# Performance work log

Hardware: AMD Instinct MI355X
Metric: run time of the kernel (lower is better)

The kernel has to match this reference:

```python
import jax, jax.numpy as jnp
import numpy as np

C = 32
KSHAPE = (C, C, 3, 3)  # (C_out, C_in, kH, kW)
BN_EPS = 1e-5


def _binary_act(x):
    # forward: sign(x); backward: identity clipped to |x|<1 (STE)
    xc = jnp.clip(x, -1.0, 1.0)
    return jax.lax.stop_gradient(jnp.sign(x) - xc) + xc


def _binarize_weight(w_flat, shape):
    w = w_flat.reshape(shape)
    scale = jax.lax.stop_gradient(jnp.mean(jnp.abs(w)))  # global scalar scale, detached
    wc = jnp.clip(w, -1.0, 1.0)
    # forward: scale*sign(w); backward flows through clamp(w,-1,1)
    return jax.lax.stop_gradient(scale * jnp.sign(w) - wc) + wc


def _bi_conv_bn(x, w_flat, gamma, beta, stride):
    xb = _binary_act(x)
    w = _binarize_weight(w_flat, KSHAPE)
    y = jax.lax.conv_general_dilated(
        xb, w, window_strides=(stride, stride), padding=[(1, 1), (1, 1)],
        dimension_numbers=('NCHW', 'OIHW', 'NCHW'))
    # BatchNorm2d in training mode (batch stats, biased variance)
    m = jnp.mean(y, axis=(0, 2, 3), keepdims=True)
    v = jnp.mean((y - m) ** 2, axis=(0, 2, 3), keepdims=True)
    yhat = (y - m) * jax.lax.rsqrt(v + BN_EPS)
    return gamma.reshape(1, -1, 1, 1) * yhat + beta.reshape(1, -1, 1, 1)


def setup_inputs() -> dict:
    key = jax.random.key(0)
    k1, k2, k3 = jax.random.split(key, 3)
    return {
        'x': jax.random.normal(k1, (32, C, 160, 160), dtype=jnp.float32),
        'w1': jax.random.normal(k2, (C * C * 9, 1), dtype=jnp.float32) * 0.05,
        'gamma1': jnp.ones((C,), dtype=jnp.float32),
        'beta1': jnp.zeros((C,), dtype=jnp.float32),
        'w2': jax.random.normal(k3, (C * C * 9, 1), dtype=jnp.float32) * 0.05,
        'gamma2': jnp.ones((C,), dtype=jnp.float32),
        'beta2': jnp.zeros((C,), dtype=jnp.float32),
    }


def reference(x, w1, gamma1, beta1, w2, gamma2, beta2):
    # bireal residual block, stride=1 => skip_op is Identity
    inner = _bi_conv_bn(x, w1, gamma1, beta1, 1) + x
    out = _bi_conv_bn(inner, w2, gamma2, beta2, 1) + inner
    return out
```

## Files before the change

kernel.cpp:

```cpp
#include <hip/hip_runtime.h>
#include <stdint.h>

#define NIMG 32
#define CH 32
#define HH 160
#define WW 160
#define HWL (HH*WW)
#define PRS 164
#define PHH 162
#define PIMG (PHH*PRS)
#define NPIX (NIMG*HWL)
#define HALO_WORDS 968

#define OFF_P     0
#define OFF_P2    3400704
#define OFF_WP    (OFF_P2 + 3400704)
#define OFF_CORR  (OFF_WP + 2304)
#define OFF_SC    (OFF_CORR + 2304)
#define OFF_SB    (OFF_SC + 128)

struct StatLine {
  int s1; int pad0; unsigned long long s2; char pad[112];
};

#define AS1 __attribute__((address_space(1)))
#define AS3 __attribute__((address_space(3)))
__device__ __forceinline__ void dma16(const void* g, void* l) {
  __builtin_amdgcn_global_load_lds((const AS1 void*)g, (AS3 void*)l, 16, 0, 0);
}

__device__ __forceinline__ void conv4(const uint32_t r[3][6], const uint32_t* wsh,
                                      int co, int& a0, int& a1, int& a2, int& a3)
{
  a0 = a1 = a2 = a3 = 0;
  #pragma unroll
  for (int dy = 0; dy < 3; ++dy) {
    #pragma unroll
    for (int dx = 0; dx < 3; ++dx) {
      uint32_t wvv = wsh[co * 9 + dy * 3 + dx];
      a0 += __popc(r[dy][0 + dx] ^ wvv);
      a1 += __popc(r[dy][1 + dx] ^ wvv);
      a2 += __popc(r[dy][2 + dx] ^ wvv);
      a3 += __popc(r[dy][3 + dx] ^ wvv);
    }
  }
}

__global__ __launch_bounds__(256) void pack_prep(const float* __restrict__ x,
    const float* __restrict__ w1, const float* __restrict__ w2,
    uint32_t* __restrict__ P, uint32_t* __restrict__ P2, uint32_t* __restrict__ WP,
    int* __restrict__ CORR, float* __restrict__ SC, StatLine* __restrict__ SB)
{
  __shared__ float lds[8192];
  const int tid = threadIdx.x;
  const int b = blockIdx.x;

  if (b >= 3200) {
    if (b == 3442) {
      int* z = (int*)SB;
      for (int i = tid; i < 2048; i += 256) z[i] = 0;
      float* red = lds;
      uint32_t* wpl = (uint32_t*)(lds + 256);
      for (int cv = 0; cv < 2; ++cv) {
        const float* w = cv ? w2 : w1;
        float s = 0.f;
        #pragma unroll
        for (int j = 0; j < 9; ++j) {
          float4 v = *reinterpret_cast<const float4*>(w + (j * 256 + tid) * 4);
          s += fabsf(v.x) + fabsf(v.y) + fabsf(v.z) + fabsf(v.w);
        }
        red[tid] = s;
        __syncthreads();
        for (int st = 128; st > 0; st >>= 1) {
          if (tid < st) red[tid] += red[tid + st];
          __syncthreads();
        }
        if (tid == 0) SC[cv] = red[0] / 9216.0f;
        for (int i = tid; i < 288; i += 256) {
          int co = i / 9, t = i - co * 9;
          uint32_t bw = 0;
          for (int ci = 0; ci < 32; ++ci)
            bw |= (w[(co * 32 + ci) * 9 + t] > 0.0f) ? (1u << ci) : 0u;
          WP[cv * 288 + i] = bw;
          wpl[i] = bw;
        }
        __syncthreads();
        for (int i = tid; i < 288; i += 256) {
          int cls = i / 32, co = i - cls * 32;
          int hc = cls / 3, wc = cls - hc * 3;
          int corr = 0;
          for (int t = 0; t < 9; ++t) {
            int dy = t / 3 - 1, dx = t % 3 - 1;
            bool inval = (hc == 0 && dy == -1) || (hc == 2 && dy == 1) ||
                         (wc == 0 && dx == -1) || (wc == 2 && dx == 1);
            if (inval) corr += 32 - 2 * __popc(wpl[co * 9 + t]);
          }
          CORR[cv * 288 + cls * 32 + co] = corr;
        }
        __syncthreads();
      }
    } else {
      int k = (b - 3200) * 256 + tid;
      uint32_t* buf = (k < 32 * HALO_WORDS) ? P : P2;
      int j = k % (32 * HALO_WORDS);
      int img = j / HALO_WORDS;
      int r = j - img * HALO_WORDS;
      int pr, pc;
      if (r < 164)      { pr = 0;   pc = r; }
      else if (r < 328) { pr = 161; pc = r - 164; }
      else {
        int k2 = r - 328;
        pr = 1 + (k2 >> 2);
        int q = k2 & 3;
        pc = (q == 0) ? 0 : (160 + q);
      }
      buf[img * PIMG + pr * PRS + pc] = 0;
    }
    return;
  }

  int n = b / 100;
  int p0 = (b - n * 100) * 256;
  const float* xb = x + (size_t)n * CH * HWL + p0;
  #pragma unroll
  for (int it = 0; it < 8; ++it) {
    int c = it * 4 + (tid >> 6);
    dma16(xb + (size_t)c * HWL + (tid & 63) * 4, lds + c * 256);
  }
  __syncthreads();

  uint32_t bits = 0;
  #pragma unroll
  for (int c = 0; c < 32; ++c) {
    if (lds[c * 256 + tid] > 0.f) bits |= 1u << c;
  }
  int px = p0 + tid;
  int h = px / WW, w = px - h * WW;
  P[n * PIMG + (h + 1) * PRS + (w + 1)] = bits;
}

__global__ __launch_bounds__(256) void conv_stats(const uint32_t* __restrict__ P,
    const uint32_t* __restrict__ WP, const int* __restrict__ CORR,
    StatLine* __restrict__ sb)
{
  __shared__ uint32_t wsh[288];
  __shared__ int csh[288];
  __shared__ int ls1[32], ls2[32];
  const int tid = threadIdx.x;
  for (int i = tid; i < 288; i += 256) { wsh[i] = WP[i]; csh[i] = CORR[i]; }
  if (tid < 32) { ls1[tid] = 0; ls2[tid] = 0; }
  __syncthreads();

  int g = blockIdx.x * 256 + tid;
  int w4 = g % 40;
  int t1 = g / 40;
  int h = t1 % 160;
  int n = t1 / 160;

  const uint32_t* base = P + n * PIMG + h * PRS + w4 * 4;
  uint32_t r[3][6];
  #pragma unroll
  for (int dy = 0; dy < 3; ++dy) {
    uint4 a = *reinterpret_cast<const uint4*>(base + dy * PRS);
    uint2 bw = *reinterpret_cast<const uint2*>(base + dy * PRS + 4);
    r[dy][0] = a.x; r[dy][1] = a.y; r[dy][2] = a.z; r[dy][3] = a.w;
    r[dy][4] = bw.x; r[dy][5] = bw.y;
  }

  int rowc = (h == 0) ? 0 : ((h == 159) ? 6 : 3);
  int cls0  = rowc + ((w4 == 0) ? 0 : 1);
  int cls12 = rowc + 1;
  int cls3  = rowc + ((w4 == 39) ? 2 : 1);
  int lane = tid & 63;

  #pragma unroll
  for (int co = 0; co < 32; ++co) {
    int a0, a1, a2, a3;
    conv4(r, wsh, co, a0, a1, a2, a3);
    int d0 = 288 - 2 * a0 - csh[cls0 * 32 + co];
    int d1 = 288 - 2 * a1 - csh[cls12 * 32 + co];
    int d2 = 288 - 2 * a2 - csh[cls12 * 32 + co];
    int d3 = 288 - 2 * a3 - csh[cls3 * 32 + co];
    int ds = d0 + d1 + d2 + d3;
    int sq = d0 * d0 + d1 * d1 + d2 * d2 + d3 * d3;
    #pragma unroll
    for (int off = 32; off > 0; off >>= 1) {
      ds += __shfl_down(ds, off);
      sq += __shfl_down(sq, off);
    }
    if (lane == 0) { atomicAdd(&ls1[co], ds); atomicAdd(&ls2[co], sq); }
  }
  __syncthreads();
  if (tid < 32) {
    atomicAdd(&sb[tid].s1, ls1[tid]);
    atomicAdd(&sb[tid].s2, (unsigned long long)(long long)ls2[tid]);
  }
}

__global__ __launch_bounds__(256, 2) void conv_bn1(const uint32_t* __restrict__ P,
    const uint32_t* __restrict__ WP, const int* __restrict__ CORR,
    const float* __restrict__ x, const float* __restrict__ SCp,
    const StatLine* __restrict__ sb, const float* __restrict__ gamma,
    const float* __restrict__ beta, uint32_t* __restrict__ P2)
{
  __shared__ uint32_t wsh[288];
  __shared__ int csh[288];
  __shared__ float Ash[32], Bsh[32];
  const int tid = threadIdx.x;
  for (int i = tid; i < 288; i += 256) { wsh[i] = WP[i]; csh[i] = CORR[i]; }
  if (tid < 32) {
    double sc = (double)SCp[0];
    double m  = sc * (double)sb[tid].s1 / (double)NPIX;
    double ms = sc * sc * (double)(long long)sb[tid].s2 / (double)NPIX;
    float inv = (float)(1.0 / sqrt(ms - m * m + 1e-5));
    float gm = gamma[tid];
    Ash[tid] = gm * inv * (float)sc;
    Bsh[tid] = beta[tid] - gm * inv * (float)m;
  }
  __syncthreads();

  int g = blockIdx.x * 256 + tid;
  int w4 = g % 40;
  int t1 = g / 40;
  int h = t1 % 160;
  int n = t1 / 160;

  const uint32_t* base = P + n * PIMG + h * PRS + w4 * 4;
  uint32_t r[3][6];
  #pragma unroll
  for (int dy = 0; dy < 3; ++dy) {
    uint4 a = *reinterpret_cast<const uint4*>(base + dy * PRS);
    uint2 bw = *reinterpret_cast<const uint2*>(base + dy * PRS + 4);
    r[dy][0] = a.x; r[dy][1] = a.y; r[dy][2] = a.z; r[dy][3] = a.w;
    r[dy][4] = bw.x; r[dy][5] = bw.y;
  }
  int rowc = (h == 0) ? 0 : ((h == 159) ? 6 : 3);
  int cls0  = rowc + ((w4 == 0) ? 0 : 1);
  int cls12 = rowc + 1;
  int cls3  = rowc + ((w4 == 39) ? 2 : 1);

  int i = h * WW + w4 * 4;
  size_t pbase = (size_t)n * CH * HWL + i;

  uint32_t bb0 = 0, bb1 = 0, bb2 = 0, bb3 = 0;
  #pragma unroll
  for (int cg = 0; cg < 4; ++cg) {
    float4 xv[8];
    #pragma unroll
    for (int j = 0; j < 8; ++j)
      xv[j] = *reinterpret_cast<const float4*>(x + pbase + (size_t)(cg * 8 + j) * HWL);
    #pragma unroll
    for (int j = 0; j < 8; ++j) {
      int co = cg * 8 + j;
      int a0, a1, a2, a3;
      conv4(r, wsh, co, a0, a1, a2, a3);
      int d0 = 288 - 2 * a0 - csh[cls0 * 32 + co];
      int d1 = 288 - 2 * a1 - csh[cls12 * 32 + co];
      int d2 = 288 - 2 * a2 - csh[cls12 * 32 + co];
      int d3 = 288 - 2 * a3 - csh[cls3 * 32 + co];
      float A = Ash[co], Bv = Bsh[co];
      float v0 = fmaf(A, (float)d0, Bv) + xv[j].x;
      float v1 = fmaf(A, (float)d1, Bv) + xv[j].y;
      float v2 = fmaf(A, (float)d2, Bv) + xv[j].z;
      float v3 = fmaf(A, (float)d3, Bv) + xv[j].w;
      uint32_t m = 1u << co;
      if (v0 > 0.f) bb0 |= m;
      if (v1 > 0.f) bb1 |= m;
      if (v2 > 0.f) bb2 |= m;
      if (v3 > 0.f) bb3 |= m;
    }
  }
  uint32_t* pw = P2 + n * PIMG + (h + 1) * PRS + (w4 * 4 + 1);
  pw[0] = bb0; pw[1] = bb1; pw[2] = bb2; pw[3] = bb3;
}

__global__ __launch_bounds__(256, 2) void conv_bn2(const uint32_t* __restrict__ P,
    const uint32_t* __restrict__ P2, const uint32_t* __restrict__ WP,
    const int* __restrict__ CORR, const float* __restrict__ x,
    const float* __restrict__ SC, const StatLine* __restrict__ SB,
    const float* __restrict__ g1v, const float* __restrict__ b1v,
    const float* __restrict__ g2v, const float* __restrict__ b2v,
    float* __restrict__ out)
{
  __shared__ uint32_t wsh[576];
  __shared__ int csh[576];
  __shared__ float A1s[32], B1s[32], A2s[32], B2s[32];
  const int tid = threadIdx.x;
  for (int i = tid; i < 576; i += 256) { wsh[i] = WP[i]; csh[i] = CORR[i]; }
  if (tid < 32) {
    double sc = (double)SC[0];
    double m  = sc * (double)SB[tid].s1 / (double)NPIX;
    double ms = sc * sc * (double)(long long)SB[tid].s2 / (double)NPIX;
    float inv = (float)(1.0 / sqrt(ms - m * m + 1e-5));
    float gm = g1v[tid];
    A1s[tid] = gm * inv * (float)sc;
    B1s[tid] = b1v[tid] - gm * inv * (float)m;
    double sc2 = (double)SC[1];
    double m2  = sc2 * (double)SB[32 + tid].s1 / (double)NPIX;
    double ms2 = sc2 * sc2 * (double)(long long)SB[32 + tid].s2 / (double)NPIX;
    float inv2 = (float)(1.0 / sqrt(ms2 - m2 * m2 + 1e-5));
    float gm2 = g2v[tid];
    A2s[tid] = gm2 * inv2 * (float)sc2;
    B2s[tid] = b2v[tid] - gm2 * inv2 * (float)m2;
  }
  __syncthreads();

  int g = blockIdx.x * 256 + tid;
  int w4 = g % 40;
  int t1 = g / 40;
  int h = t1 % 160;
  int n = t1 / 160;

  uint32_t r1[3][6], r2[3][6];
  {
    const uint32_t* b1p = P  + n * PIMG + h * PRS + w4 * 4;
    const uint32_t* b2p = P2 + n * PIMG + h * PRS + w4 * 4;
    #pragma unroll
    for (int dy = 0; dy < 3; ++dy) {
      uint4 a = *reinterpret_cast<const uint4*>(b1p + dy * PRS);
      uint2 bw = *reinterpret_cast<const uint2*>(b1p + dy * PRS + 4);
      r1[dy][0] = a.x; r1[dy][1] = a.y; r1[dy][2] = a.z; r1[dy][3] = a.w;
      r1[dy][4] = bw.x; r1[dy][5] = bw.y;
      uint4 c = *reinterpret_cast<const uint4*>(b2p + dy * PRS);
      uint2 dw = *reinterpret_cast<const uint2*>(b2p + dy * PRS + 4);
      r2[dy][0] = c.x; r2[dy][1] = c.y; r2[dy][2] = c.z; r2[dy][3] = c.w;
      r2[dy][4] = dw.x; r2[dy][5] = dw.y;
    }
  }
  int rowc = (h == 0) ? 0 : ((h == 159) ? 6 : 3);
  int cls0  = rowc + ((w4 == 0) ? 0 : 1);
  int cls12 = rowc + 1;
  int cls3  = rowc + ((w4 == 39) ? 2 : 1);

  int i = h * WW + w4 * 4;
  size_t pbase = (size_t)n * CH * HWL + i;

  #pragma unroll
  for (int cg = 0; cg < 4; ++cg) {
    float4 xv[8];
    #pragma unroll
    for (int j = 0; j < 8; ++j)
      xv[j] = *reinterpret_cast<const float4*>(x + pbase + (size_t)(cg * 8 + j) * HWL);
    #pragma unroll
    for (int j = 0; j < 8; ++j) {
      int co = cg * 8 + j;
      int a0, a1, a2, a3, e0, e1, e2, e3;
      conv4(r1, wsh, co, a0, a1, a2, a3);
      conv4(r2, wsh + 288, co, e0, e1, e2, e3);
      int d0 = 288 - 2 * a0 - csh[cls0 * 32 + co];
      int d1 = 288 - 2 * a1 - csh[cls12 * 32 + co];
      int d2 = 288 - 2 * a2 - csh[cls12 * 32 + co];
      int d3 = 288 - 2 * a3 - csh[cls3 * 32 + co];
      int f0 = 288 - 2 * e0 - csh[288 + cls0 * 32 + co];
      int f1 = 288 - 2 * e1 - csh[288 + cls12 * 32 + co];
      int f2 = 288 - 2 * e2 - csh[288 + cls12 * 32 + co];
      int f3 = 288 - 2 * e3 - csh[288 + cls3 * 32 + co];
      float A1 = A1s[co], B1 = B1s[co], A2 = A2s[co], B2 = B2s[co];
      float v0 = fmaf(A1, (float)d0, B1) + xv[j].x;
      float v1 = fmaf(A1, (float)d1, B1) + xv[j].y;
      float v2 = fmaf(A1, (float)d2, B1) + xv[j].z;
      float v3 = fmaf(A1, (float)d3, B1) + xv[j].w;
      float4 o;
      o.x = fmaf(A2, (float)f0, B2) + v0;
      o.y = fmaf(A2, (float)f1, B2) + v1;
      o.z = fmaf(A2, (float)f2, B2) + v2;
      o.w = fmaf(A2, (float)f3, B2) + v3;
      *reinterpret_cast<float4*>(out + pbase + (size_t)co * HWL) = o;
    }
  }
}

extern "C" void kernel_launch(void* const* d_in, const int* in_sizes, int n_in,
                              void* d_out, int out_size, void* d_ws, size_t ws_size,
                              hipStream_t stream)
{
  (void)in_sizes; (void)n_in; (void)out_size; (void)ws_size;
  const float* x  = (const float*)d_in[0];
  const float* w1 = (const float*)d_in[1];
  const float* g1 = (const float*)d_in[2];
  const float* b1 = (const float*)d_in[3];
  const float* w2 = (const float*)d_in[4];
  const float* g2 = (const float*)d_in[5];
  const float* b2 = (const float*)d_in[6];
  float* out = (float*)d_out;
  char* ws = (char*)d_ws;

  uint32_t* P    = (uint32_t*)(ws + OFF_P);
  uint32_t* P2   = (uint32_t*)(ws + OFF_P2);
  uint32_t* WP   = (uint32_t*)(ws + OFF_WP);
  int*      CORR = (int*)(ws + OFF_CORR);
  float*    SC   = (float*)(ws + OFF_SC);
  StatLine* SB   = (StatLine*)(ws + OFF_SB);

  pack_prep<<<3443, 256, 0, stream>>>(x, w1, w2, P, P2, WP, CORR, SC, SB);
  conv_stats<<<800, 256, 0, stream>>>(P, WP, CORR, SB);
  conv_bn1<<<800, 256, 0, stream>>>(P, WP, CORR, x, SC, SB, g1, b1, P2);
  conv_stats<<<800, 256, 0, stream>>>(P2, WP + 288, CORR + 288, SB + 32);
  conv_bn2<<<800, 256, 0, stream>>>(P, P2, WP, CORR, x, SC, SB, g1, b1, g2, b2, out);
}
```

Before: 194.7 us.

## Store int16 conv results in stats pass instead of recomputing binary convs

The stats passes now write the integer conv outputs of both binary convolutions as int16 to new workspace buffers Y1 and Y2. The bn1 and final kernels then read these values instead of recomputing the popcount convolutions, so the final kernel no longer redoes two convolutions. This trades XNOR/popcount compute for extra HBM traffic: about 52 MB written per conv and re-read up to twice, on top of the existing fp32 x reads and output writes.

```diff
diff --git a/kernel.cpp b/kernel.cpp
--- a/kernel.cpp
+++ b/kernel.cpp
@@ -14,7 +14,9 @@
 
 #define OFF_P     0
 #define OFF_P2    3400704
-#define OFF_WP    (OFF_P2 + 3400704)
+#define OFF_Y1    (OFF_P2 + 3400704)
+#define OFF_Y2    (OFF_Y1 + 52428800)
+#define OFF_WP    (OFF_Y2 + 52428800)
 #define OFF_CORR  (OFF_WP + 2304)
 #define OFF_SC    (OFF_CORR + 2304)
 #define OFF_SB    (OFF_SC + 128)
@@ -44,6 +46,18 @@
       a3 += __popc(r[dy][3 + dx] ^ wvv);
     }
   }
+}
+
+__device__ __forceinline__ void bn_affine(const float* SCp, const StatLine* sb,
+    const float* gamma, const float* beta, int c, float& A, float& B)
+{
+  double sc = (double)SCp[0];
+  double m  = sc * (double)sb[c].s1 / (double)NPIX;
+  double ms = sc * sc * (double)(long long)sb[c].s2 / (double)NPIX;
+  float inv = (float)(1.0 / sqrt(ms - m * m + 1e-5));
+  float gm = gamma[c];
+  A = gm * inv * (float)sc;
+  B = beta[c] - gm * inv * (float)m;
 }
 
 __global__ __launch_bounds__(256) void pack_prep(const float* __restrict__ x,
@@ -139,9 +153,9 @@
   P[n * PIMG + (h + 1) * PRS + (w + 1)] = bits;
 }
 
-__global__ __launch_bounds__(256) void conv_stats(const uint32_t* __restrict__ P,
+__global__ __launch_bounds__(256) void conv_stats_y(const uint32_t* __restrict__ P,
     const uint32_t* __restrict__ WP, const int* __restrict__ CORR,
-    StatLine* __restrict__ sb)
+    short* __restrict__ Y, StatLine* __restrict__ sb)
 {
   __shared__ uint32_t wsh[288];
   __shared__ int csh[288];
@@ -172,6 +186,8 @@
   int cls12 = rowc + 1;
   int cls3  = rowc + ((w4 == 39) ? 2 : 1);
   int lane = tid & 63;
+
+  short* yb = Y + (size_t)n * CH * HWL + h * WW + w4 * 4;
 
   #pragma unroll
   for (int co = 0; co < 32; ++co) {
@@ -181,6 +197,8 @@
     int d1 = 288 - 2 * a1 - csh[cls12 * 32 + co];
     int d2 = 288 - 2 * a2 - csh[cls12 * 32 + co];
     int d3 = 288 - 2 * a3 - csh[cls3 * 32 + co];
+    *reinterpret_cast<short4*>(yb + (size_t)co * HWL) =
+        make_short4((short)d0, (short)d1, (short)d2, (short)d3);
     int ds = d0 + d1 + d2 + d3;
     int sq = d0 * d0 + d1 * d1 + d2 * d2 + d3 * d3;
     #pragma unroll
@@ -197,26 +215,14 @@
   }
 }
 
-__global__ __launch_bounds__(256, 2) void conv_bn1(const uint32_t* __restrict__ P,
-    const uint32_t* __restrict__ WP, const int* __restrict__ CORR,
+__global__ __launch_bounds__(256, 2) void bits2(const short* __restrict__ Y1,
     const float* __restrict__ x, const float* __restrict__ SCp,
     const StatLine* __restrict__ sb, const float* __restrict__ gamma,
     const float* __restrict__ beta, uint32_t* __restrict__ P2)
 {
-  __shared__ uint32_t wsh[288];
-  __shared__ int csh[288];
   __shared__ float Ash[32], Bsh[32];
   const int tid = threadIdx.x;
-  for (int i = tid; i < 288; i += 256) { wsh[i] = WP[i]; csh[i] = CORR[i]; }
-  if (tid < 32) {
-    double sc = (double)SCp[0];
-    double m  = sc * (double)sb[tid].s1 / (double)NPIX;
-    double ms = sc * sc * (double)(long long)sb[tid].s2 / (double)NPIX;
-    float inv = (float)(1.0 / sqrt(ms - m * m + 1e-5));
-    float gm = gamma[tid];
-    Ash[tid] = gm * inv * (float)sc;
-    Bsh[tid] = beta[tid] - gm * inv * (float)m;
-  }
+  if (tid < 32) bn_affine(SCp, sb, gamma, beta, tid, Ash[tid], Bsh[tid]);
   __syncthreads();
 
   int g = blockIdx.x * 256 + tid;
@@ -224,21 +230,6 @@
   int t1 = g / 40;
   int h = t1 % 160;
   int n = t1 / 160;
-
-  const uint32_t* base = P + n * PIMG + h * PRS + w4 * 4;
-  uint32_t r[3][6];
-  #pragma unroll
-  for (int dy = 0; dy < 3; ++dy) {
-    uint4 a = *reinterpret_cast<const uint4*>(base + dy * PRS);
-    uint2 bw = *reinterpret_cast<const uint2*>(base + dy * PRS + 4);
-    r[dy][0] = a.x; r[dy][1] = a.y; r[dy][2] = a.z; r[dy][3] = a.w;
-    r[dy][4] = bw.x; r[dy][5] = bw.y;
-  }
-  int rowc = (h == 0) ? 0 : ((h == 159) ? 6 : 3);
-  int cls0  = rowc + ((w4 == 0) ? 0 : 1);
-  int cls12 = rowc + 1;
-  int cls3  = rowc + ((w4 == 39) ? 2 : 1);
-
   int i = h * WW + w4 * 4;
   size_t pbase = (size_t)n * CH * HWL + i;
 
@@ -246,23 +237,21 @@
   #pragma unroll
   for (int cg = 0; cg < 4; ++cg) {
     float4 xv[8];
-    #pragma unroll
-    for (int j = 0; j < 8; ++j)
-      xv[j] = *reinterpret_cast<const float4*>(x + pbase + (size_t)(cg * 8 + j) * HWL);
+    short4 yv[8];
+    #pragma unroll
+    for (int j = 0; j < 8; ++j) {
+      size_t idx = pbase + (size_t)(cg * 8 + j) * HWL;
+      xv[j] = *reinterpret_cast<const float4*>(x + idx);
+      yv[j] = *reinterpret_cast<const short4*>(Y1 + idx);
+    }
     #pragma unroll
     for (int j = 0; j < 8; ++j) {
       int co = cg * 8 + j;
-      int a0, a1, a2, a3;
-      conv4(r, wsh, co, a0, a1, a2, a3);
-      int d0 = 288 - 2 * a0 - csh[cls0 * 32 + co];
-      int d1 = 288 - 2 * a1 - csh[cls12 * 32 + co];
-      int d2 = 288 - 2 * a2 - csh[cls12 * 32 + co];
-      int d3 = 288 - 2 * a3 - csh[cls3 * 32 + co];
       float A = Ash[co], Bv = Bsh[co];
-      float v0 = fmaf(A, (float)d0, Bv) + xv[j].x;
-      float v1 = fmaf(A, (float)d1, Bv) + xv[j].y;
-      float v2 = fmaf(A, (float)d2, Bv) + xv[j].z;
-      float v3 = fmaf(A, (float)d3, Bv) + xv[j].w;
+      float v0 = fmaf(A, (float)yv[j].x, Bv) + xv[j].x;
+      float v1 = fmaf(A, (float)yv[j].y, Bv) + xv[j].y;
+      float v2 = fmaf(A, (float)yv[j].z, Bv) + xv[j].z;
+      float v3 = fmaf(A, (float)yv[j].w, Bv) + xv[j].w;
       uint32_t m = 1u << co;
       if (v0 > 0.f) bb0 |= m;
       if (v1 > 0.f) bb1 |= m;
@@ -274,34 +263,18 @@
   pw[0] = bb0; pw[1] = bb1; pw[2] = bb2; pw[3] = bb3;
 }
 
-__global__ __launch_bounds__(256, 2) void conv_bn2(const uint32_t* __restrict__ P,
-    const uint32_t* __restrict__ P2, const uint32_t* __restrict__ WP,
-    const int* __restrict__ CORR, const float* __restrict__ x,
+__global__ __launch_bounds__(256, 2) void bnout(const short* __restrict__ Y1,
+    const short* __restrict__ Y2, const float* __restrict__ x,
     const float* __restrict__ SC, const StatLine* __restrict__ SB,
     const float* __restrict__ g1v, const float* __restrict__ b1v,
     const float* __restrict__ g2v, const float* __restrict__ b2v,
     float* __restrict__ out)
 {
-  __shared__ uint32_t wsh[576];
-  __shared__ int csh[576];
   __shared__ float A1s[32], B1s[32], A2s[32], B2s[32];
   const int tid = threadIdx.x;
-  for (int i = tid; i < 576; i += 256) { wsh[i] = WP[i]; csh[i] = CORR[i]; }
   if (tid < 32) {
-    double sc = (double)SC[0];
-    double m  = sc * (double)SB[tid].s1 / (double)NPIX;
-    double ms = sc * sc * (double)(long long)SB[tid].s2 / (double)NPIX;
-    float inv = (float)(1.0 / sqrt(ms - m * m + 1e-5));
-    float gm = g1v[tid];
-    A1s[tid] = gm * inv * (float)sc;
-    B1s[tid] = b1v[tid] - gm * inv * (float)m;
-    double sc2 = (double)SC[1];
-    double m2  = sc2 * (double)SB[32 + tid].s1 / (double)NPIX;
-    double ms2 = sc2 * sc2 * (double)(long long)SB[32 + tid].s2 / (double)NPIX;
-    float inv2 = (float)(1.0 / sqrt(ms2 - m2 * m2 + 1e-5));
-    float gm2 = g2v[tid];
-    A2s[tid] = gm2 * inv2 * (float)sc2;
-    B2s[tid] = b2v[tid] - gm2 * inv2 * (float)m2;
+    bn_affine(SC, SB, g1v, b1v, tid, A1s[tid], B1s[tid]);
+    bn_affine(SC + 1, SB + 32, g2v, b2v, tid, A2s[tid], B2s[tid]);
   }
   __syncthreads();
 
@@ -310,61 +283,33 @@
   int t1 = g / 40;
   int h = t1 % 160;
   int n = t1 / 160;
-
-  uint32_t r1[3][6], r2[3][6];
-  {
-    const uint32_t* b1p = P  + n * PIMG + h * PRS + w4 * 4;
-    const uint32_t* b2p = P2 + n * PIMG + h * PRS + w4 * 4;
-    #pragma unroll
-    for (int dy = 0; dy < 3; ++dy) {
-      uint4 a = *reinterpret_cast<const uint4*>(b1p + dy * PRS);
-      uint2 bw = *reinterpret_cast<const uint2*>(b1p + dy * PRS + 4);
-      r1[dy][0] = a.x; r1[dy][1] = a.y; r1[dy][2] = a.z; r1[dy][3] = a.w;
-      r1[dy][4] = bw.x; r1[dy][5] = bw.y;
-      uint4 c = *reinterpret_cast<const uint4*>(b2p + dy * PRS);
-      uint2 dw = *reinterpret_cast<const uint2*>(b2p + dy * PRS + 4);
-      r2[dy][0] = c.x; r2[dy][1] = c.y; r2[dy][2] = c.z; r2[dy][3] = c.w;
-      r2[dy][4] = dw.x; r2[dy][5] = dw.y;
-    }
-  }
-  int rowc = (h == 0) ? 0 : ((h == 159) ? 6 : 3);
-  int cls0  = rowc + ((w4 == 0) ? 0 : 1);
-  int cls12 = rowc + 1;
-  int cls3  = rowc + ((w4 == 39) ? 2 : 1);
-
   int i = h * WW + w4 * 4;
   size_t pbase = (size_t)n * CH * HWL + i;
 
   #pragma unroll
   for (int cg = 0; cg < 4; ++cg) {
     float4 xv[8];
-    #pragma unroll
-    for (int j = 0; j < 8; ++j)
-      xv[j] = *reinterpret_cast<const float4*>(x + pbase + (size_t)(cg * 8 + j) * HWL);
+    short4 y1v[8], y2v[8];
+    #pragma unroll
+    for (int j = 0; j < 8; ++j) {
+      size_t idx = pbase + (size_t)(cg * 8 + j) * HWL;
+      xv[j]  = *reinterpret_cast<const float4*>(x + idx);
+      y1v[j] = *reinterpret_cast<const short4*>(Y1 + idx);
+      y2v[j] = *reinterpret_cast<const short4*>(Y2 + idx);
+    }
     #pragma unroll
     for (int j = 0; j < 8; ++j) {
       int co = cg * 8 + j;
-      int a0, a1, a2, a3, e0, e1, e2, e3;
-      conv4(r1, wsh, co, a0, a1, a2, a3);
-      conv4(r2, wsh + 288, co, e0, e1, e2, e3);
-      int d0 = 288 - 2 * a0 - csh[cls0 * 32 + co];
-      int d1 = 288 - 2 * a1 - csh[cls12 * 32 + co];
-      int d2 = 288 - 2 * a2 - csh[cls12 * 32 + co];
-      int d3 = 288 - 2 * a3 - csh[cls3 * 32 + co];
-      int f0 = 288 - 2 * e0 - csh[288 + cls0 * 32 + co];
-      int f1 = 288 - 2 * e1 - csh[288 + cls12 * 32 + co];
-      int f2 = 288 - 2 * e2 - csh[288 + cls12 * 32 + co];
-      int f3 = 288 - 2 * e3 - csh[288 + cls3 * 32 + co];
       float A1 = A1s[co], B1 = B1s[co], A2 = A2s[co], B2 = B2s[co];
-      float v0 = fmaf(A1, (float)d0, B1) + xv[j].x;
-      float v1 = fmaf(A1, (float)d1, B1) + xv[j].y;
-      float v2 = fmaf(A1, (float)d2, B1) + xv[j].z;
-      float v3 = fmaf(A1, (float)d3, B1) + xv[j].w;
+      float v0 = fmaf(A1, (float)y1v[j].x, B1) + xv[j].x;
+      float v1 = fmaf(A1, (float)y1v[j].y, B1) + xv[j].y;
+      float v2 = fmaf(A1, (float)y1v[j].z, B1) + xv[j].z;
+      float v3 = fmaf(A1, (float)y1v[j].w, B1) + xv[j].w;
       float4 o;
-      o.x = fmaf(A2, (float)f0, B2) + v0;
-      o.y = fmaf(A2, (float)f1, B2) + v1;
-      o.z = fmaf(A2, (float)f2, B2) + v2;
-      o.w = fmaf(A2, (float)f3, B2) + v3;
+      o.x = fmaf(A2, (float)y2v[j].x, B2) + v0;
+      o.y = fmaf(A2, (float)y2v[j].y, B2) + v1;
+      o.z = fmaf(A2, (float)y2v[j].z, B2) + v2;
+      o.w = fmaf(A2, (float)y2v[j].w, B2) + v3;
       *reinterpret_cast<float4*>(out + pbase + (size_t)co * HWL) = o;
     }
   }
@@ -387,14 +332,16 @@
 
   uint32_t* P    = (uint32_t*)(ws + OFF_P);
   uint32_t* P2   = (uint32_t*)(ws + OFF_P2);
+  short*    Y1   = (short*)(ws + OFF_Y1);
+  short*    Y2   = (short*)(ws + OFF_Y2);
   uint32_t* WP   = (uint32_t*)(ws + OFF_WP);
   int*      CORR = (int*)(ws + OFF_CORR);
   float*    SC   = (float*)(ws + OFF_SC);
   StatLine* SB   = (StatLine*)(ws + OFF_SB);
 
   pack_prep<<<3443, 256, 0, stream>>>(x, w1, w2, P, P2, WP, CORR, SC, SB);
-  conv_stats<<<800, 256, 0, stream>>>(P, WP, CORR, SB);
-  conv_bn1<<<800, 256, 0, stream>>>(P, WP, CORR, x, SC, SB, g1, b1, P2);
-  conv_stats<<<800, 256, 0, stream>>>(P2, WP + 288, CORR + 288, SB + 32);
-  conv_bn2<<<800, 256, 0, stream>>>(P, P2, WP, CORR, x, SC, SB, g1, b1, g2, b2, out);
-}
+  conv_stats_y<<<800, 256, 0, stream>>>(P, WP, CORR, Y1, SB);
+  bits2<<<800, 256, 0, stream>>>(Y1, x, SC, SB, g1, b1, P2);
+  conv_stats_y<<<800, 256, 0, stream>>>(P2, WP + 288, CORR + 288, Y2, SB + 32);
+  bnout<<<800, 256, 0, stream>>>(Y1, Y2, x, SC, SB, g1, b1, g2, b2, out);
+}
```

Result: slower. 207.8 us (+6.7%).
